# Optimization experiments

Hardware: AMD Instinct MI355X
Metric: run time of the kernel (lower is better)

Reference implementation:

```python
import jax, jax.numpy as jnp
import numpy as np

NB_LAYERS, KSIZE = 4, 5
DILATIONS = [1, 2, 4, 8]
NEG_SLOPE = 0.1
BN_EPS = 1e-5


def _cont_conv(times, feats, mask, dilation, p):
    """One ContConv1d layer: causal gather of time-diffs -> kernel MLP -> weighted aggregate + skip + BN."""
    k1W, k1b, k2W, k2b, k3W, k3b, skipW, skipb, gamma, beta = p
    bs, L, Cin = feats.shape
    Cout = skipW.shape[1]
    lags = jnp.arange(KSIZE) * dilation                    # (K,) include_zero_lag=True -> lag 0 included
    idx = jnp.arange(L)[None, :] - lags[:, None]           # (K, L) causal neighbor indices
    valid = idx >= 0
    idx_c = jnp.clip(idx, 0, L - 1)
    g_times = times[:, idx_c]                              # (bs, K, L)
    g_feats = feats[:, idx_c, :]                           # (bs, K, L, Cin)
    g_mask = (mask[:, idx_c] & valid[None] & mask[:, None, :]).astype(feats.dtype)
    dt = (times[:, None, :] - g_times) * g_mask            # (bs, K, L) zeroed where invalid
    # kernel MLP: scalar time-diff -> (Cin, Cout) mixing matrix
    h = jax.nn.leaky_relu(dt[..., None] @ k1W + k1b, NEG_SLOPE)
    h = jax.nn.leaky_relu(h @ k2W + k2b, NEG_SLOPE)
    kv = (h @ k3W + k3b).reshape(bs, KSIZE, L, Cin, Cout) * g_mask[..., None, None]
    out = jnp.einsum('bklc,bklcd->bld', g_feats, kv)       # aggregate over taps and input channels
    out = out + feats @ skipW + skipb                      # 1x1-conv skip connection
    mu = out.mean((0, 1))                                  # BatchNorm1d (training-mode batch stats)
    var = out.var((0, 1))
    return (out - mu) * jax.lax.rsqrt(var + BN_EPS) * gamma + beta


def _ccnn_forward(event_times, event_types, emb, k1W, k1b, k2W, k2b, k3W, k3b, skipW, skipb, gamma, beta):
    bs = event_times.shape[0]
    emb = emb.at[0].set(0.0)                               # padding_idx = 0
    times = jnp.concatenate([jnp.zeros((bs, 1), event_times.dtype), event_times], axis=1)
    bos = jnp.full((bs, 1), jnp.max(event_types) + 1, dtype=event_types.dtype)
    types = jnp.concatenate([bos, event_types], axis=1)
    mask = times != 0                                      # BOS (t=0) masked, as in the original
    enc = emb[types]                                       # (bs, L+1, C)
    for i in range(NB_LAYERS):
        p = (k1W[i], k1b[i], k2W[i], k2b[i], k3W[i], k3b[i], skipW[i], skipb[i], gamma[i], beta[i])
        enc = jax.nn.leaky_relu(_cont_conv(times, enc, mask, DILATIONS[i], p), NEG_SLOPE)
    return enc


def setup_inputs() -> dict:
    key = jax.random.key(0)
    ks = jax.random.split(key, 12)
    bs, L, C, H, num_types = 8, 2048, 32, 16, 100
    s = 0.05
    gaps = jax.random.uniform(ks[0], (bs, L)) * 0.1 + 0.01
    times = jnp.cumsum(gaps, axis=1)                       # strictly increasing positive event times
    types = jax.random.randint(ks[1], (bs, L), 0, num_types) + 1   # 1..num_types
    pad = jnp.arange(L) >= int(0.9 * L)
    times = jnp.where(pad[None, :], 0.0, times).astype(jnp.float32)
    types = jnp.where(pad[None, :], 0, types).astype(jnp.int32)
    return {
        'event_times': times,
        'event_types': types,
        'emb': jax.random.normal(ks[2], (num_types + 2, C)) * s,
        'k1W': jax.random.normal(ks[3], (NB_LAYERS, 1, H)) * s,
        'k1b': jnp.zeros((NB_LAYERS, H)),
        'k2W': jax.random.normal(ks[4], (NB_LAYERS, H, H)) * s,
        'k2b': jnp.zeros((NB_LAYERS, H)),
        'k3W': jax.random.normal(ks[5], (NB_LAYERS, H, C * C)) * s,
        'k3b': jnp.zeros((NB_LAYERS, C * C)),
        'skipW': jax.random.normal(ks[6], (NB_LAYERS, C, C)) * s,
        'skipb': jnp.zeros((NB_LAYERS, C)),
        'gamma': jnp.ones((NB_LAYERS, C)),
        'beta': jnp.zeros((NB_LAYERS, C)),
    }


def reference(event_times, event_types, emb, k1W, k1b, k2W, k2b, k3W, k3b, skipW, skipb, gamma, beta):
    return _ccnn_forward(event_times, event_types, emb, k1W, k1b, k2W, k2b, k3W, k3b, skipW, skipb, gamma, beta)
```

## Files before the change

kernel.cpp:

```cpp
#include <hip/hip_runtime.h>
#include <stdint.h>

#define NB_LAYERS 4
#define KSIZE 5
#define BSZ 8
#define LIN 2048
#define LSEQ 2049
#define CCH 32
#define HCH 16
#define MROWS (BSZ*LSEQ)
#define NTILES ((MROWS+15)/16)
#define KDIM 576
#define NEG 0.1f
#define BNEPS 1e-5f
#define NWAVEMAX 256

typedef _Float16 h2v __attribute__((ext_vector_type(2)));
typedef _Float16 h8v __attribute__((ext_vector_type(8)));
typedef float    f4v __attribute__((ext_vector_type(4)));

union H8 { h8v v; h2v h[4]; };

static __device__ __forceinline__ h2v mkh2(float a, float b) {
  h2v r; r[0] = (_Float16)a; r[1] = (_Float16)b; return r;
}

__global__ __launch_bounds__(256) void prep_kernel(
    const float* __restrict__ k3W, const float* __restrict__ k3b,
    const float* __restrict__ skipW, _Float16* __restrict__ Wt,
    const int* __restrict__ types, int* __restrict__ wavemax,
    float* __restrict__ stats) {
  int id = blockIdx.x * blockDim.x + threadIdx.x;

  if (id < NB_LAYERS * 64) stats[id] = 0.f;

  if (id < BSZ * LIN) {
    int v = types[id];
#pragma unroll
    for (int off = 32; off; off >>= 1) v = max(v, __shfl_xor(v, off, 64));
    if ((threadIdx.x & 63) == 0) wavemax[id >> 6] = v;
  }

  {
    int layer = id / (CCH * KDIM);
    int rem = id % (CCH * KDIM);
    int n = rem / KDIM;
    int k = rem % KDIM;
    float val;
    if (k < 512)      { int h = k >> 5, c = k & 31; val = k3W[layer*16384 + h*1024 + c*32 + n]; }
    else if (k < 544) { int c = k - 512;            val = k3b[layer*1024 + c*32 + n]; }
    else              { int c = k - 544;            val = skipW[layer*1024 + c*32 + n]; }
    Wt[id] = (_Float16)val;
  }
}

__global__ __launch_bounds__(256) void embed_kernel(
    const int* __restrict__ types, const float* __restrict__ emb,
    const int* __restrict__ wavemax, float* __restrict__ enc) {
  int id = blockIdx.x * blockDim.x + threadIdx.x;
  int row = id >> 5, c = id & 31;
  int b = row / LSEQ, pos = row % LSEQ;
  int t;
  if (pos == 0) {
    const int4* wm = (const int4*)wavemax;
    int mx = 0;
    for (int i = 0; i < NWAVEMAX / 4; i++) {
      int4 v = wm[i];
      mx = max(mx, max(max(v.x, v.y), max(v.z, v.w)));
    }
    t = mx + 1;
  } else {
    t = types[b * LIN + pos - 1];
  }
  enc[id] = (t == 0) ? 0.f : emb[t * CCH + c];
}

template<bool FUSE_BN>
__global__ __launch_bounds__(256) void conv_kernel(
    const float* __restrict__ enc_in, float* __restrict__ enc_out,
    const float* __restrict__ etimes,
    const float* __restrict__ k1Wp, const float* __restrict__ k1bp,
    const float* __restrict__ k2Wp, const float* __restrict__ k2bp,
    const _Float16* __restrict__ Wt,
    const float* __restrict__ stats_prev, float* __restrict__ stats_out,
    const float* __restrict__ gamma_prev, const float* __restrict__ beta_prev,
    int dil)
{
  __shared__ float sst[64];
  if (threadIdx.x < 64) sst[threadIdx.x] = 0.f;
  __syncthreads();

  const int lane = threadIdx.x & 63;
  const int wv   = threadIdx.x >> 6;
  const int m    = lane & 15;
  const int q    = lane >> 4;

  float k1w[HCH], k1b[HCH], k2b[HCH];
#pragma unroll
  for (int h = 0; h < HCH; h++) { k1w[h] = k1Wp[h]; k1b[h] = k1bp[h]; k2b[h] = k2bp[h]; }

  float sc8[8], ob8[8];
  if (FUSE_BN) {
    const float inv = 1.f / (float)MROWS;
#pragma unroll
    for (int j = 0; j < 8; j++) {
      int c = q * 8 + j;
      float mu = stats_prev[c] * inv;
      float var = stats_prev[32 + c] * inv - mu * mu;
      float sc = gamma_prev[c] * rsqrtf(var + BNEPS);
      sc8[j] = sc; ob8[j] = beta_prev[c] - mu * sc;
    }
  }

  const _Float16* wb0 = Wt + m * KDIM + q * 8;
  const _Float16* wb1 = Wt + (m + 16) * KDIM + q * 8;

  const int tile = blockIdx.x * 4 + wv;
  {
    int row = tile * 16 + m;
    bool rvalid = row < MROWS;
    int rowc = min(row, MROWS - 1);
    int b = rowc / LSEQ, pos = rowc % LSEQ;
    float t_l = (pos == 0) ? 0.f : etimes[b * LIN + pos - 1];
    bool mask_l = rvalid && (t_l != 0.f);

    h2v wh[KSIZE][8];
    h2v fh[KSIZE][4];
    h2v fself[4];
    float Fb[8];
#pragma unroll
    for (int jj = 0; jj < 8; jj++) Fb[jj] = 0.f;

#pragma unroll
    for (int tap = 0; tap < KSIZE; tap++) {
      int j = pos - tap * dil;
      int jc = max(j, 0);
      float t_j = (jc == 0) ? 0.f : etimes[b * LIN + jc - 1];
      bool gm = mask_l && (j >= 0) && (t_j != 0.f);
      float dt = gm ? (t_l - t_j) : 0.f;

      const float* fp = enc_in + (b * LSEQ + jc) * CCH + q * 8;
      float4 fA = *(const float4*)(fp);
      float4 fB = *(const float4*)(fp + 4);
      float fv[8] = {fA.x, fA.y, fA.z, fA.w, fB.x, fB.y, fB.z, fB.w};
      if (FUSE_BN) {
#pragma unroll
        for (int jj = 0; jj < 8; jj++) {
          float x = fmaf(fv[jj], sc8[jj], ob8[jj]);
          fv[jj] = fmaxf(x, NEG * x);
        }
      }

      if (tap == 0) {
        float rv = rvalid ? 1.f : 0.f;
#pragma unroll
        for (int p2 = 0; p2 < 4; p2++) fself[p2] = mkh2(fv[2*p2] * rv, fv[2*p2+1] * rv);
      }
      float g = gm ? 1.f : 0.f;
#pragma unroll
      for (int jj = 0; jj < 8; jj++) Fb[jj] += g * fv[jj];
#pragma unroll
      for (int p2 = 0; p2 < 4; p2++) fh[tap][p2] = mkh2(fv[2*p2], fv[2*p2+1]);

      if (__ballot(gm)) {
        float h1[HCH];
#pragma unroll
        for (int h = 0; h < HCH; h++) { float x = fmaf(dt, k1w[h], k1b[h]); h1[h] = fmaxf(x, NEG * x); }
        float h2[HCH];
#pragma unroll
        for (int h = 0; h < HCH; h++) h2[h] = k2b[h];
#pragma unroll
        for (int hp = 0; hp < HCH; hp++) {
          float hv = h1[hp];
#pragma unroll
          for (int h = 0; h < HCH; h++) h2[h] = fmaf(hv, k2Wp[hp * HCH + h], h2[h]);
        }
#pragma unroll
        for (int hh = 0; hh < 8; hh++) {
          float a = h2[2*hh];     a = fmaxf(a, NEG * a) * g;
          float c2 = h2[2*hh+1];  c2 = fmaxf(c2, NEG * c2) * g;
          wh[tap][hh] = mkh2(a, c2);
        }
      } else {
#pragma unroll
        for (int hh = 0; hh < 8; hh++) wh[tap][hh] = mkh2(0.f, 0.f);
      }
    }

    f4v acc0 = {0.f, 0.f, 0.f, 0.f};
    f4v acc1 = {0.f, 0.f, 0.f, 0.f};

#pragma unroll
    for (int ks = 0; ks < 16; ks++) {
      H8 bf0, bf1, af;
      bf0.v = *(const h8v*)(wb0 + ks * 32);
      bf1.v = *(const h8v*)(wb1 + ks * 32);
      h2v u0 = mkh2(0.f,0.f), u1 = mkh2(0.f,0.f), u2 = mkh2(0.f,0.f), u3 = mkh2(0.f,0.f);
#pragma unroll
      for (int tap = 0; tap < KSIZE; tap++) {
        _Float16 w = wh[tap][ks >> 1][ks & 1];
        h2v wd; wd[0] = w; wd[1] = w;
        u0 += wd * fh[tap][0];
        u1 += wd * fh[tap][1];
        u2 += wd * fh[tap][2];
        u3 += wd * fh[tap][3];
      }
      af.h[0] = u0; af.h[1] = u1; af.h[2] = u2; af.h[3] = u3;
      acc0 = __builtin_amdgcn_mfma_f32_16x16x32_f16(af.v, bf0.v, acc0, 0, 0, 0);
      acc1 = __builtin_amdgcn_mfma_f32_16x16x32_f16(af.v, bf1.v, acc1, 0, 0, 0);
    }
    {
      H8 bf0, bf1, af;
      bf0.v = *(const h8v*)(wb0 + 512);
      bf1.v = *(const h8v*)(wb1 + 512);
#pragma unroll
      for (int p2 = 0; p2 < 4; p2++) af.h[p2] = mkh2(Fb[2*p2], Fb[2*p2+1]);
      acc0 = __builtin_amdgcn_mfma_f32_16x16x32_f16(af.v, bf0.v, acc0, 0, 0, 0);
      acc1 = __builtin_amdgcn_mfma_f32_16x16x32_f16(af.v, bf1.v, acc1, 0, 0, 0);
    }
    {
      H8 bf0, bf1, af;
      bf0.v = *(const h8v*)(wb0 + 544);
      bf1.v = *(const h8v*)(wb1 + 544);
      af.h[0] = fself[0]; af.h[1] = fself[1]; af.h[2] = fself[2]; af.h[3] = fself[3];
      acc0 = __builtin_amdgcn_mfma_f32_16x16x32_f16(af.v, bf0.v, acc0, 0, 0, 0);
      acc1 = __builtin_amdgcn_mfma_f32_16x16x32_f16(af.v, bf1.v, acc1, 0, 0, 0);
    }

    float s0 = 0.f, s1 = 0.f, s2 = 0.f, s3 = 0.f;
#pragma unroll
    for (int r = 0; r < 4; r++) {
      float v0 = acc0[r], v1 = acc1[r];
      s0 += v0; s1 += v0 * v0; s2 += v1; s3 += v1 * v1;
      int rd = tile * 16 + q * 4 + r;
      if (rd < MROWS) {
        enc_out[rd * CCH + m] = v0;
        enc_out[rd * CCH + 16 + m] = v1;
      }
    }
    s0 += __shfl_xor(s0, 16, 64); s0 += __shfl_xor(s0, 32, 64);
    s1 += __shfl_xor(s1, 16, 64); s1 += __shfl_xor(s1, 32, 64);
    s2 += __shfl_xor(s2, 16, 64); s2 += __shfl_xor(s2, 32, 64);
    s3 += __shfl_xor(s3, 16, 64); s3 += __shfl_xor(s3, 32, 64);
    if (q == 0) {
      atomicAdd(&sst[m], s0);
      atomicAdd(&sst[32 + m], s1);
      atomicAdd(&sst[16 + m], s2);
      atomicAdd(&sst[48 + m], s3);
    }
  }
  __syncthreads();
  if (threadIdx.x < 64) atomicAdd(&stats_out[threadIdx.x], sst[threadIdx.x]);
}

__global__ __launch_bounds__(256) void bn_kernel(
    const float* __restrict__ x, float* __restrict__ out,
    const float* __restrict__ stats,
    const float* __restrict__ gamma, const float* __restrict__ beta) {
  int id = blockIdx.x * blockDim.x + threadIdx.x;
  int c = id & 31;
  const float inv = 1.f / (float)MROWS;
  float mu = stats[c] * inv;
  float var = stats[32 + c] * inv - mu * mu;
  float sc = gamma[c] * rsqrtf(var + BNEPS);
  float v = fmaf(x[id], sc, beta[c] - mu * sc);
  out[id] = fmaxf(v, NEG * v);
}

extern "C" void kernel_launch(void* const* d_in, const int* in_sizes, int n_in,
                              void* d_out, int out_size, void* d_ws, size_t ws_size,
                              hipStream_t stream) {
  (void)in_sizes; (void)n_in; (void)out_size; (void)ws_size;
  const float* event_times = (const float*)d_in[0];
  const int*   event_types = (const int*)d_in[1];
  const float* emb   = (const float*)d_in[2];
  const float* k1W   = (const float*)d_in[3];
  const float* k1b   = (const float*)d_in[4];
  const float* k2W   = (const float*)d_in[5];
  const float* k2b   = (const float*)d_in[6];
  const float* k3W   = (const float*)d_in[7];
  const float* k3b   = (const float*)d_in[8];
  const float* skipW = (const float*)d_in[9];
  const float* gamma = (const float*)d_in[11];
  const float* beta  = (const float*)d_in[12];

  float* enc_a = (float*)d_ws;
  float* enc_b = enc_a + (size_t)MROWS * CCH;
  float* stats = enc_b + (size_t)MROWS * CCH;
  int*   wavemax = (int*)(stats + NB_LAYERS * 64);
  _Float16* Wt = (_Float16*)(((uintptr_t)(wavemax + NWAVEMAX) + 255) & ~(uintptr_t)255);

  prep_kernel<<<288, 256, 0, stream>>>(k3W, k3b, skipW, Wt, event_types, wavemax, stats);
  embed_kernel<<<2049, 256, 0, stream>>>(event_types, emb, wavemax, enc_a);

  conv_kernel<false><<<257, 256, 0, stream>>>(enc_a, enc_b, event_times,
      k1W, k1b, k2W, k2b, Wt, nullptr, stats, nullptr, nullptr, 1);
  const int dils[NB_LAYERS] = {1, 2, 4, 8};
  const float* bufs[2] = {enc_a, enc_b};
  for (int i = 1; i < NB_LAYERS; i++) {
    const float* cin = bufs[i & 1];
    float* cout = (float*)bufs[(i + 1) & 1];
    conv_kernel<true><<<257, 256, 0, stream>>>(cin, cout, event_times,
        k1W + i * HCH, k1b + i * HCH, k2W + i * HCH * HCH, k2b + i * HCH,
        Wt + (size_t)i * CCH * KDIM,
        stats + (i - 1) * 64, stats + i * 64,
        gamma + (i - 1) * CCH, beta + (i - 1) * CCH, dils[i]);
  }
  bn_kernel<<<2049, 256, 0, stream>>>(enc_a, (float*)d_out,
      stats + 3 * 64, gamma + 3 * CCH, beta + 3 * CCH);
}
```

Before: 166.7 us.

## Fuse embedding into first conv layer and split kernel-MLP work across lanes via LDS

Removes the separate embedding kernel by gathering embedding rows directly inside the first conv layer (MODE 0), which skips writing and re-reading the full encoded tensor once. The per-tap kernel MLP, previously run redundantly by all four lane quarters for every tap, is now spread so each lane quarter computes one tap (plus a second pass for the fifth tap), with results exchanged through shared memory. MLP weights are staged in LDS, and the block size changes to 320 threads (5 waves) with a grid of 205 blocks. This adds an extra barrier and LDS traffic, and the fifth-tap pass runs on only a quarter of the lanes.

```diff
diff --git a/kernel.cpp b/kernel.cpp
--- a/kernel.cpp
+++ b/kernel.cpp
@@ -14,6 +14,8 @@
 #define NEG 0.1f
 #define BNEPS 1e-5f
 #define NWAVEMAX 256
+#define CONVGRID 205
+#define CONVBLK 320
 
 typedef _Float16 h2v __attribute__((ext_vector_type(2)));
 typedef _Float16 h8v __attribute__((ext_vector_type(8)));
@@ -54,30 +56,13 @@
   }
 }
 
-__global__ __launch_bounds__(256) void embed_kernel(
-    const int* __restrict__ types, const float* __restrict__ emb,
-    const int* __restrict__ wavemax, float* __restrict__ enc) {
-  int id = blockIdx.x * blockDim.x + threadIdx.x;
-  int row = id >> 5, c = id & 31;
-  int b = row / LSEQ, pos = row % LSEQ;
-  int t;
-  if (pos == 0) {
-    const int4* wm = (const int4*)wavemax;
-    int mx = 0;
-    for (int i = 0; i < NWAVEMAX / 4; i++) {
-      int4 v = wm[i];
-      mx = max(mx, max(max(v.x, v.y), max(v.z, v.w)));
-    }
-    t = mx + 1;
-  } else {
-    t = types[b * LIN + pos - 1];
-  }
-  enc[id] = (t == 0) ? 0.f : emb[t * CCH + c];
-}
-
-template<bool FUSE_BN>
-__global__ __launch_bounds__(256) void conv_kernel(
-    const float* __restrict__ enc_in, float* __restrict__ enc_out,
+template<int MODE>
+__global__ __launch_bounds__(CONVBLK) void conv_kernel(
+    const float* __restrict__ enc_in,
+    const int*   __restrict__ types,
+    const float* __restrict__ emb,
+    const int*   __restrict__ wavemax,
+    float* __restrict__ enc_out,
     const float* __restrict__ etimes,
     const float* __restrict__ k1Wp, const float* __restrict__ k1bp,
     const float* __restrict__ k2Wp, const float* __restrict__ k2bp,
@@ -87,20 +72,22 @@
     int dil)
 {
   __shared__ float sst[64];
-  if (threadIdx.x < 64) sst[threadIdx.x] = 0.f;
-  __syncthreads();
-
-  const int lane = threadIdx.x & 63;
-  const int wv   = threadIdx.x >> 6;
+  __shared__ alignas(16) float sW[304];
+  __shared__ h8v swh[CONVBLK/64 * KSIZE * 16 * 2];
+
+  const int tid  = threadIdx.x;
+  const int lane = tid & 63;
+  const int wv   = tid >> 6;
   const int m    = lane & 15;
   const int q    = lane >> 4;
 
-  float k1w[HCH], k1b[HCH], k2b[HCH];
-#pragma unroll
-  for (int h = 0; h < HCH; h++) { k1w[h] = k1Wp[h]; k1b[h] = k1bp[h]; k2b[h] = k2bp[h]; }
+  if (tid < 64) sst[tid] = 0.f;
+  if (tid < 16) { sW[tid] = k1Wp[tid]; sW[16 + tid] = k1bp[tid]; sW[32 + tid] = k2bp[tid]; }
+  if (tid >= 64 && tid < 64 + 256) sW[48 + tid - 64] = k2Wp[tid - 64];
+  __syncthreads();
 
   float sc8[8], ob8[8];
-  if (FUSE_BN) {
+  if (MODE == 1) {
     const float inv = 1.f / (float)MROWS;
 #pragma unroll
     for (int j = 0; j < 8; j++) {
@@ -115,142 +102,207 @@
   const _Float16* wb0 = Wt + m * KDIM + q * 8;
   const _Float16* wb1 = Wt + (m + 16) * KDIM + q * 8;
 
-  const int tile = blockIdx.x * 4 + wv;
-  {
-    int row = tile * 16 + m;
-    bool rvalid = row < MROWS;
-    int rowc = min(row, MROWS - 1);
-    int b = rowc / LSEQ, pos = rowc % LSEQ;
-    float t_l = (pos == 0) ? 0.f : etimes[b * LIN + pos - 1];
-    bool mask_l = rvalid && (t_l != 0.f);
-
-    h2v wh[KSIZE][8];
-    h2v fh[KSIZE][4];
-    h2v fself[4];
-    float Fb[8];
-#pragma unroll
-    for (int jj = 0; jj < 8; jj++) Fb[jj] = 0.f;
-
-#pragma unroll
-    for (int tap = 0; tap < KSIZE; tap++) {
-      int j = pos - tap * dil;
-      int jc = max(j, 0);
-      float t_j = (jc == 0) ? 0.f : etimes[b * LIN + jc - 1];
-      bool gm = mask_l && (j >= 0) && (t_j != 0.f);
-      float dt = gm ? (t_l - t_j) : 0.f;
-
+  const int tile = blockIdx.x * (CONVBLK / 64) + wv;
+  int row = tile * 16 + m;
+  bool rvalid = row < MROWS;
+  int rowc = min(row, MROWS - 1);
+  int b = rowc / LSEQ, pos = rowc % LSEQ;
+  float t_l = (pos == 0) ? 0.f : etimes[b * LIN + pos - 1];
+  bool mask_l = rvalid && (t_l != 0.f);
+
+  int bosv = 0;
+  if (MODE == 0) {
+    if (__ballot(pos == 0)) {
+      const int4* wm = (const int4*)wavemax;
+      int mx = 0;
+#pragma unroll 4
+      for (int i = 0; i < NWAVEMAX / 4; i++) {
+        int4 v = wm[i];
+        mx = max(mx, max(max(v.x, v.y), max(v.z, v.w)));
+      }
+      bosv = mx + 1;
+    }
+  }
+
+  h2v fh[KSIZE][4];
+  h2v fself[4];
+  float Fb[8];
+#pragma unroll
+  for (int jj = 0; jj < 8; jj++) Fb[jj] = 0.f;
+
+#pragma unroll
+  for (int tap = 0; tap < KSIZE; tap++) {
+    int j = pos - tap * dil;
+    int jc = max(j, 0);
+    float t_j = (jc == 0) ? 0.f : etimes[b * LIN + jc - 1];
+    bool gm = mask_l && (j >= 0) && (t_j != 0.f);
+
+    float fv[8];
+    if (MODE == 0) {
+      int tl = 0;
+      if (jc > 0) tl = types[b * LIN + jc - 1];
+      int t = (jc == 0) ? ((tap == 0) ? bosv : 0) : tl;
+      const float* ep = emb + t * CCH + q * 8;
+      float4 eA = *(const float4*)(ep);
+      float4 eB = *(const float4*)(ep + 4);
+      float zf = (t != 0) ? 1.f : 0.f;
+      fv[0]=eA.x*zf; fv[1]=eA.y*zf; fv[2]=eA.z*zf; fv[3]=eA.w*zf;
+      fv[4]=eB.x*zf; fv[5]=eB.y*zf; fv[6]=eB.z*zf; fv[7]=eB.w*zf;
+    } else {
       const float* fp = enc_in + (b * LSEQ + jc) * CCH + q * 8;
       float4 fA = *(const float4*)(fp);
       float4 fB = *(const float4*)(fp + 4);
-      float fv[8] = {fA.x, fA.y, fA.z, fA.w, fB.x, fB.y, fB.z, fB.w};
-      if (FUSE_BN) {
-#pragma unroll
-        for (int jj = 0; jj < 8; jj++) {
-          float x = fmaf(fv[jj], sc8[jj], ob8[jj]);
-          fv[jj] = fmaxf(x, NEG * x);
+      fv[0]=fA.x; fv[1]=fA.y; fv[2]=fA.z; fv[3]=fA.w;
+      fv[4]=fB.x; fv[5]=fB.y; fv[6]=fB.z; fv[7]=fB.w;
+#pragma unroll
+      for (int jj = 0; jj < 8; jj++) {
+        float x = fmaf(fv[jj], sc8[jj], ob8[jj]);
+        fv[jj] = fmaxf(x, NEG * x);
+      }
+    }
+
+    if (tap == 0) {
+      float rv = rvalid ? 1.f : 0.f;
+#pragma unroll
+      for (int p2 = 0; p2 < 4; p2++) fself[p2] = mkh2(fv[2*p2] * rv, fv[2*p2+1] * rv);
+    }
+    float g = gm ? 1.f : 0.f;
+#pragma unroll
+    for (int jj = 0; jj < 8; jj++) Fb[jj] += g * fv[jj];
+#pragma unroll
+    for (int p2 = 0; p2 < 4; p2++) fh[tap][p2] = mkh2(fv[2*p2], fv[2*p2+1]);
+  }
+
+#pragma unroll
+  for (int rep = 0; rep < 2; rep++) {
+    const int jt = rep ? (KSIZE - 1) : (lane >> 4);
+    const bool act = rep ? (lane < 16) : true;
+    int j2 = pos - jt * dil;
+    int jc2 = max(j2, 0);
+    float tj2 = (jc2 == 0) ? 0.f : etimes[b * LIN + jc2 - 1];
+    bool g2 = act && mask_l && (j2 >= 0) && (tj2 != 0.f);
+    float dt = g2 ? (t_l - tj2) : 0.f;
+
+    H8 w0, w1;
+    if (__ballot(g2)) {
+      const f4v* k1wv = (const f4v*)&sW[0];
+      const f4v* k1bv = (const f4v*)&sW[16];
+      const f4v* k2bv = (const f4v*)&sW[32];
+      float h1[HCH], h2[HCH];
+#pragma unroll
+      for (int h4 = 0; h4 < 4; h4++) {
+        f4v cw = k1wv[h4], cb = k1bv[h4], c2 = k2bv[h4];
+#pragma unroll
+        for (int r = 0; r < 4; r++) {
+          float x = fmaf(dt, cw[r], cb[r]);
+          h1[h4*4+r] = fmaxf(x, NEG * x);
+          h2[h4*4+r] = c2[r];
         }
       }
-
-      if (tap == 0) {
-        float rv = rvalid ? 1.f : 0.f;
-#pragma unroll
-        for (int p2 = 0; p2 < 4; p2++) fself[p2] = mkh2(fv[2*p2] * rv, fv[2*p2+1] * rv);
-      }
-      float g = gm ? 1.f : 0.f;
-#pragma unroll
-      for (int jj = 0; jj < 8; jj++) Fb[jj] += g * fv[jj];
-#pragma unroll
-      for (int p2 = 0; p2 < 4; p2++) fh[tap][p2] = mkh2(fv[2*p2], fv[2*p2+1]);
-
-      if (__ballot(gm)) {
-        float h1[HCH];
-#pragma unroll
-        for (int h = 0; h < HCH; h++) { float x = fmaf(dt, k1w[h], k1b[h]); h1[h] = fmaxf(x, NEG * x); }
-        float h2[HCH];
-#pragma unroll
-        for (int h = 0; h < HCH; h++) h2[h] = k2b[h];
-#pragma unroll
-        for (int hp = 0; hp < HCH; hp++) {
-          float hv = h1[hp];
-#pragma unroll
-          for (int h = 0; h < HCH; h++) h2[h] = fmaf(hv, k2Wp[hp * HCH + h], h2[h]);
+#pragma unroll
+      for (int hp = 0; hp < HCH; hp++) {
+        float hv = h1[hp];
+        const f4v* kk = (const f4v*)&sW[48 + hp * 16];
+#pragma unroll
+        for (int h4 = 0; h4 < 4; h4++) {
+          f4v c = kk[h4];
+#pragma unroll
+          for (int r = 0; r < 4; r++) h2[h4*4+r] = fmaf(hv, c[r], h2[h4*4+r]);
         }
-#pragma unroll
-        for (int hh = 0; hh < 8; hh++) {
-          float a = h2[2*hh];     a = fmaxf(a, NEG * a) * g;
-          float c2 = h2[2*hh+1];  c2 = fmaxf(c2, NEG * c2) * g;
-          wh[tap][hh] = mkh2(a, c2);
-        }
-      } else {
-#pragma unroll
-        for (int hh = 0; hh < 8; hh++) wh[tap][hh] = mkh2(0.f, 0.f);
-      }
-    }
-
-    f4v acc0 = {0.f, 0.f, 0.f, 0.f};
-    f4v acc1 = {0.f, 0.f, 0.f, 0.f};
-
-#pragma unroll
-    for (int ks = 0; ks < 16; ks++) {
-      H8 bf0, bf1, af;
-      bf0.v = *(const h8v*)(wb0 + ks * 32);
-      bf1.v = *(const h8v*)(wb1 + ks * 32);
-      h2v u0 = mkh2(0.f,0.f), u1 = mkh2(0.f,0.f), u2 = mkh2(0.f,0.f), u3 = mkh2(0.f,0.f);
-#pragma unroll
-      for (int tap = 0; tap < KSIZE; tap++) {
-        _Float16 w = wh[tap][ks >> 1][ks & 1];
-        h2v wd; wd[0] = w; wd[1] = w;
-        u0 += wd * fh[tap][0];
-        u1 += wd * fh[tap][1];
-        u2 += wd * fh[tap][2];
-        u3 += wd * fh[tap][3];
-      }
-      af.h[0] = u0; af.h[1] = u1; af.h[2] = u2; af.h[3] = u3;
-      acc0 = __builtin_amdgcn_mfma_f32_16x16x32_f16(af.v, bf0.v, acc0, 0, 0, 0);
-      acc1 = __builtin_amdgcn_mfma_f32_16x16x32_f16(af.v, bf1.v, acc1, 0, 0, 0);
-    }
-    {
-      H8 bf0, bf1, af;
-      bf0.v = *(const h8v*)(wb0 + 512);
-      bf1.v = *(const h8v*)(wb1 + 512);
-#pragma unroll
-      for (int p2 = 0; p2 < 4; p2++) af.h[p2] = mkh2(Fb[2*p2], Fb[2*p2+1]);
-      acc0 = __builtin_amdgcn_mfma_f32_16x16x32_f16(af.v, bf0.v, acc0, 0, 0, 0);
-      acc1 = __builtin_amdgcn_mfma_f32_16x16x32_f16(af.v, bf1.v, acc1, 0, 0, 0);
-    }
-    {
-      H8 bf0, bf1, af;
-      bf0.v = *(const h8v*)(wb0 + 544);
-      bf1.v = *(const h8v*)(wb1 + 544);
-      af.h[0] = fself[0]; af.h[1] = fself[1]; af.h[2] = fself[2]; af.h[3] = fself[3];
-      acc0 = __builtin_amdgcn_mfma_f32_16x16x32_f16(af.v, bf0.v, acc0, 0, 0, 0);
-      acc1 = __builtin_amdgcn_mfma_f32_16x16x32_f16(af.v, bf1.v, acc1, 0, 0, 0);
-    }
-
-    float s0 = 0.f, s1 = 0.f, s2 = 0.f, s3 = 0.f;
-#pragma unroll
-    for (int r = 0; r < 4; r++) {
-      float v0 = acc0[r], v1 = acc1[r];
-      s0 += v0; s1 += v0 * v0; s2 += v1; s3 += v1 * v1;
-      int rd = tile * 16 + q * 4 + r;
-      if (rd < MROWS) {
-        enc_out[rd * CCH + m] = v0;
-        enc_out[rd * CCH + 16 + m] = v1;
-      }
-    }
-    s0 += __shfl_xor(s0, 16, 64); s0 += __shfl_xor(s0, 32, 64);
-    s1 += __shfl_xor(s1, 16, 64); s1 += __shfl_xor(s1, 32, 64);
-    s2 += __shfl_xor(s2, 16, 64); s2 += __shfl_xor(s2, 32, 64);
-    s3 += __shfl_xor(s3, 16, 64); s3 += __shfl_xor(s3, 32, 64);
-    if (q == 0) {
-      atomicAdd(&sst[m], s0);
-      atomicAdd(&sst[32 + m], s1);
-      atomicAdd(&sst[16 + m], s2);
-      atomicAdd(&sst[48 + m], s3);
+      }
+      float g = g2 ? 1.f : 0.f;
+#pragma unroll
+      for (int p2 = 0; p2 < 4; p2++) {
+        float a0 = h2[2*p2];     a0 = fmaxf(a0, NEG * a0) * g;
+        float a1 = h2[2*p2+1];   a1 = fmaxf(a1, NEG * a1) * g;
+        w0.h[p2] = mkh2(a0, a1);
+        float b0 = h2[8+2*p2];   b0 = fmaxf(b0, NEG * b0) * g;
+        float b1 = h2[8+2*p2+1]; b1 = fmaxf(b1, NEG * b1) * g;
+        w1.h[p2] = mkh2(b0, b1);
+      }
+    } else {
+#pragma unroll
+      for (int p2 = 0; p2 < 4; p2++) { w0.h[p2] = mkh2(0.f, 0.f); w1.h[p2] = mkh2(0.f, 0.f); }
+    }
+    if (act) {
+      int base = ((wv * KSIZE + jt) * 16 + m) * 2;
+      swh[base] = w0.v; swh[base + 1] = w1.v;
     }
   }
   __syncthreads();
-  if (threadIdx.x < 64) atomicAdd(&stats_out[threadIdx.x], sst[threadIdx.x]);
+
+  h2v wh[KSIZE][8];
+#pragma unroll
+  for (int tap = 0; tap < KSIZE; tap++) {
+    int base = ((wv * KSIZE + tap) * 16 + m) * 2;
+    H8 a0, a1; a0.v = swh[base]; a1.v = swh[base + 1];
+#pragma unroll
+    for (int p2 = 0; p2 < 4; p2++) { wh[tap][p2] = a0.h[p2]; wh[tap][4+p2] = a1.h[p2]; }
+  }
+
+  f4v acc0 = {0.f, 0.f, 0.f, 0.f};
+  f4v acc1 = {0.f, 0.f, 0.f, 0.f};
+
+#pragma unroll
+  for (int ks = 0; ks < 16; ks++) {
+    H8 bf0, bf1, af;
+    bf0.v = *(const h8v*)(wb0 + ks * 32);
+    bf1.v = *(const h8v*)(wb1 + ks * 32);
+    h2v u0 = mkh2(0.f,0.f), u1 = mkh2(0.f,0.f), u2 = mkh2(0.f,0.f), u3 = mkh2(0.f,0.f);
+#pragma unroll
+    for (int tap = 0; tap < KSIZE; tap++) {
+      _Float16 w = wh[tap][ks >> 1][ks & 1];
+      h2v wd; wd[0] = w; wd[1] = w;
+      u0 += wd * fh[tap][0];
+      u1 += wd * fh[tap][1];
+      u2 += wd * fh[tap][2];
+      u3 += wd * fh[tap][3];
+    }
+    af.h[0] = u0; af.h[1] = u1; af.h[2] = u2; af.h[3] = u3;
+    acc0 = __builtin_amdgcn_mfma_f32_16x16x32_f16(af.v, bf0.v, acc0, 0, 0, 0);
+    acc1 = __builtin_amdgcn_mfma_f32_16x16x32_f16(af.v, bf1.v, acc1, 0, 0, 0);
+  }
+  {
+    H8 bf0, bf1, af;
+    bf0.v = *(const h8v*)(wb0 + 512);
+    bf1.v = *(const h8v*)(wb1 + 512);
+#pragma unroll
+    for (int p2 = 0; p2 < 4; p2++) af.h[p2] = mkh2(Fb[2*p2], Fb[2*p2+1]);
+    acc0 = __builtin_amdgcn_mfma_f32_16x16x32_f16(af.v, bf0.v, acc0, 0, 0, 0);
+    acc1 = __builtin_amdgcn_mfma_f32_16x16x32_f16(af.v, bf1.v, acc1, 0, 0, 0);
+  }
+  {
+    H8 bf0, bf1, af;
+    bf0.v = *(const h8v*)(wb0 + 544);
+    bf1.v = *(const h8v*)(wb1 + 544);
+    af.h[0] = fself[0]; af.h[1] = fself[1]; af.h[2] = fself[2]; af.h[3] = fself[3];
+    acc0 = __builtin_amdgcn_mfma_f32_16x16x32_f16(af.v, bf0.v, acc0, 0, 0, 0);
+    acc1 = __builtin_amdgcn_mfma_f32_16x16x32_f16(af.v, bf1.v, acc1, 0, 0, 0);
+  }
+
+  float s0 = 0.f, s1 = 0.f, s2 = 0.f, s3 = 0.f;
+#pragma unroll
+  for (int r = 0; r < 4; r++) {
+    float v0 = acc0[r], v1 = acc1[r];
+    s0 += v0; s1 += v0 * v0; s2 += v1; s3 += v1 * v1;
+    int rd = tile * 16 + q * 4 + r;
+    if (rd < MROWS) {
+      enc_out[rd * CCH + m] = v0;
+      enc_out[rd * CCH + 16 + m] = v1;
+    }
+  }
+  s0 += __shfl_xor(s0, 16, 64); s0 += __shfl_xor(s0, 32, 64);
+  s1 += __shfl_xor(s1, 16, 64); s1 += __shfl_xor(s1, 32, 64);
+  s2 += __shfl_xor(s2, 16, 64); s2 += __shfl_xor(s2, 32, 64);
+  s3 += __shfl_xor(s3, 16, 64); s3 += __shfl_xor(s3, 32, 64);
+  if (q == 0) {
+    atomicAdd(&sst[m], s0);
+    atomicAdd(&sst[32 + m], s1);
+    atomicAdd(&sst[16 + m], s2);
+    atomicAdd(&sst[48 + m], s3);
+  }
+  __syncthreads();
+  if (tid < 64) atomicAdd(&stats_out[tid], sst[tid]);
 }
 
 __global__ __launch_bounds__(256) void bn_kernel(
@@ -291,16 +343,18 @@
   _Float16* Wt = (_Float16*)(((uintptr_t)(wavemax + NWAVEMAX) + 255) & ~(uintptr_t)255);
 
   prep_kernel<<<288, 256, 0, stream>>>(k3W, k3b, skipW, Wt, event_types, wavemax, stats);
-  embed_kernel<<<2049, 256, 0, stream>>>(event_types, emb, wavemax, enc_a);
-
-  conv_kernel<false><<<257, 256, 0, stream>>>(enc_a, enc_b, event_times,
+
+  conv_kernel<0><<<CONVGRID, CONVBLK, 0, stream>>>(
+      nullptr, event_types, emb, wavemax, enc_b, event_times,
       k1W, k1b, k2W, k2b, Wt, nullptr, stats, nullptr, nullptr, 1);
+
   const int dils[NB_LAYERS] = {1, 2, 4, 8};
-  const float* bufs[2] = {enc_a, enc_b};
+  float* bufs[2] = {enc_a, enc_b};
   for (int i = 1; i < NB_LAYERS; i++) {
     const float* cin = bufs[i & 1];
-    float* cout = (float*)bufs[(i + 1) & 1];
-    conv_kernel<true><<<257, 256, 0, stream>>>(cin, cout, event_times,
+    float* cout = bufs[(i + 1) & 1];
+    conv_kernel<1><<<CONVGRID, CONVBLK, 0, stream>>>(
+        cin, nullptr, nullptr, nullptr, cout, event_times,
         k1W + i * HCH, k1b + i * HCH, k2W + i * HCH * HCH, k2b + i * HCH,
         Wt + (size_t)i * CCH * KDIM,
         stats + (i - 1) * 64, stats + i * 64,
```

New measurement: 152.4 us. 1.09x faster.
